# Optimization experiments

Measured on AMD Instinct MI355X. Metric: run time of the kernel, lower is better.

## Reference

```python
import jax, jax.numpy as jnp
import numpy as np

H = 100          # hidden_size
D = 2 * H        # mod / q_enc feature dim (BiDAF hidden)
B, L, G, Q = 16, 2048, 12, 64
NEG = -1e30


def _bidaf(c, q, c_mask, q_mask, cw, qw, cqw, bias):
    """BiDAF attention. c:(B,Lc,D) q:(B,Q,D) -> (B,Lc,4D). Eval mode (no dropout)."""
    s0 = c @ cw                                    # (B,Lc,1)
    s1 = jnp.swapaxes(q @ qw, 1, 2)                # (B,1,Q)
    s2 = jnp.einsum('bld,bqd->blq', c * cqw, q)    # (B,Lc,Q)
    s = s0 + s1 + s2 + bias
    p_q = jax.nn.softmax(jnp.where(q_mask[:, None, :] > 0, s, NEG), axis=2)  # c2q
    p_c = jax.nn.softmax(jnp.where(c_mask[:, :, None] > 0, s, NEG), axis=1)  # q2c
    a = p_q @ q                                    # (B,Lc,D)
    qc = jnp.einsum('blq,bld->bqd', p_c, c)        # s2^T @ c, reassociated
    b2 = p_q @ qc                                  # == (p_q @ p_c^T) @ c
    return jnp.concatenate([c, a, c * a, c * b2], axis=-1)


def setup_inputs() -> dict:
    ks = jax.random.split(jax.random.key(0), 16)
    f32 = jnp.float32
    inp = {
        'att': jax.random.normal(ks[0], (B, L, 8 * H), f32),
        'mod': jax.random.normal(ks[1], (B, L, D), f32),
        'gap_indices': jax.random.randint(ks[2], (B, G), 0, L),
        'mask': jnp.ones((B, L), jnp.int32),
        'q_enc': jax.random.normal(ks[3], (B, Q, D), f32),
        'q_mask': jnp.ones((B, Q), jnp.int32),
        'c_weight': jax.random.normal(ks[4], (D, 1), f32) * 0.07,
        'q_weight': jax.random.normal(ks[5], (D, 1), f32) * 0.07,
        'cq_weight': jax.random.normal(ks[6], (1, 1, D), f32) * 0.07,
        'bidaf_bias': jnp.zeros((1,), f32),
        'w_att': jax.random.normal(ks[7], (3 * 8 * H, 1), f32) * 0.02,
        'b_att': jnp.zeros((1,), f32),
        'w_mod': jax.random.normal(ks[8], (3 * 2 * H, 1), f32) * 0.04,
        'b_mod': jnp.zeros((1,), f32),
        'w_att2': jax.random.normal(ks[9], (3 * 8 * H, 1), f32) * 0.02,
        'b_att2': jnp.zeros((1,), f32),
        'w_att_s': jax.random.normal(ks[10], (3 * 8 * H, 1), f32) * 0.02,
        'b_att_s': jnp.zeros((1,), f32),
        'w_mod_s': jax.random.normal(ks[11], (3 * 2 * H, 1), f32) * 0.04,
        'b_mod_s': jnp.zeros((1,), f32),
        'w_att_s2': jax.random.normal(ks[12], (3 * 8 * H, 1), f32) * 0.02,
        'b_att_s2': jnp.zeros((1,), f32),
    }
    return inp


def reference(att, mod, gap_indices, mask, q_enc, q_mask,
              c_weight, q_weight, cq_weight, bidaf_bias,
              w_att, b_att, w_mod, b_mod, w_att2, b_att2,
              w_att_s, b_att_s, w_mod_s, b_mod_s, w_att_s2, b_att_s2):
    Bz, Lz, _ = mod.shape
    idx_b = jnp.arange(Bz)[:, None]
    att_gaps = att[idx_b, gap_indices]            # (B,G,8H)
    mod_gaps = mod[idx_b, gap_indices]            # (B,G,2H)
    att2_gaps = _bidaf(mod_gaps, q_enc, jnp.ones_like(gap_indices), q_mask,
                       c_weight, q_weight, cq_weight, bidaf_bias)  # (B,G,8H)

    maskf = mask.astype(jnp.float32)
    cnt0 = maskf.sum(1)[:, None]                  # (B,1)
    pool0_mod = jnp.concatenate([mod.max(1), mod.sum(1) / cnt0], -1)   # (B,4H)
    pool0_att = jnp.concatenate([att.max(1), att.sum(1) / cnt0], -1)   # (B,16H)
    pool0_att2 = jnp.zeros((Bz, 2 * 8 * H), mod.dtype)                 # (B,1600)

    positions = jnp.arange(Lz)[None, :]           # (1,L)

    def step(carry, gid):                          # gid: (B,)
        wm = (positions >= gid[:, None] - 12) & (positions <= gid[:, None] + 12) & (mask > 0)
        wmf = wm.astype(jnp.float32)
        cnt = wmf.sum(1)[:, None]                  # (B,1)
        modw = mod * wmf[:, :, None]
        attw = att * wmf[:, :, None]
        pm = jnp.concatenate([modw.max(1), modw.sum(1) / cnt], -1)
        pa = jnp.concatenate([attw.max(1), attw.sum(1) / cnt], -1)
        a2 = _bidaf(modw, q_enc, wm.astype(jnp.int32), q_mask,
                    c_weight, q_weight, cq_weight, bidaf_bias)   # (B,L,8H)
        p2 = jnp.concatenate([a2.max(1), a2.sum(1) / cnt], -1)
        return carry, (pm, pa, p2)

    _, (pm, pa, p2) = jax.lax.scan(step, None, gap_indices[:, 1:].T)
    pools_mod = jnp.concatenate([pool0_mod[:, None], jnp.swapaxes(pm, 0, 1)], 1)   # (B,G,4H)
    pools_att = jnp.concatenate([pool0_att[:, None], jnp.swapaxes(pa, 0, 1)], 1)   # (B,G,16H)
    pools_att2 = jnp.concatenate([pool0_att2[:, None], jnp.swapaxes(p2, 0, 1)], 1) # (B,G,16H)

    mod_cat = jnp.concatenate([mod_gaps, pools_mod], -1)      # (B,G,6H)
    att_cat = jnp.concatenate([att_gaps, pools_att], -1)      # (B,G,24H)
    att2_cat = jnp.concatenate([att2_gaps, pools_att2], -1)   # (B,G,24H)

    logit_start = (att_cat[:, :1] @ w_att_s + b_att_s
                   + mod_cat[:, :1] @ w_mod_s + b_mod_s
                   + att2_cat[:, :1] @ w_att_s2 + b_att_s2)
    logit_rest = (att_cat[:, 1:] @ w_att + b_att
                  + mod_cat[:, 1:] @ w_mod + b_mod
                  + att2_cat[:, 1:] @ w_att2 + b_att2)
    logits = jnp.concatenate([logit_start, logit_rest], 1)[:, :, 0]   # (B,G)
    return logits
```

## Files before the change

kernel.cpp:

```cpp
#include <hip/hip_runtime.h>
#include <math.h>


constexpr int LL = 2048;
constexpr int GG = 12;
constexpr int QQ = 64;
constexpr int DD = 200;
constexpr int AD = 800;
constexpr int NW = 25;
constexpr float FNEG = -1e30f;

constexpr size_t OFF_PAM = 0;
constexpr size_t OFF_PAS = 204800;
constexpr size_t OFF_PMM = 409600;
constexpr size_t OFF_PMS = 460800;

#define IDX_QE(q, d) ((q) * 204 + (((q) >> 3) << 2) + (d))

#define DOT27(ACC, PR, V)                                                      \
  {                                                                            \
    const float4 _p0 = PR[0], _p1 = PR[1], _p2 = PR[2], _p3 = PR[3],           \
                 _p4 = PR[4], _p5 = PR[5], _p6 = PR[6];                        \
    ACC[0] += _p0.x * V;  ACC[1] += _p0.y * V;  ACC[2] += _p0.z * V;           \
    ACC[3] += _p0.w * V;  ACC[4] += _p1.x * V;  ACC[5] += _p1.y * V;           \
    ACC[6] += _p1.z * V;  ACC[7] += _p1.w * V;  ACC[8] += _p2.x * V;           \
    ACC[9] += _p2.y * V;  ACC[10] += _p2.z * V; ACC[11] += _p2.w * V;          \
    ACC[12] += _p3.x * V; ACC[13] += _p3.y * V; ACC[14] += _p3.z * V;          \
    ACC[15] += _p3.w * V; ACC[16] += _p4.x * V; ACC[17] += _p4.y * V;          \
    ACC[18] += _p4.z * V; ACC[19] += _p4.w * V; ACC[20] += _p5.x * V;          \
    ACC[21] += _p5.y * V; ACC[22] += _p5.z * V; ACC[23] += _p5.w * V;          \
    ACC[24] += _p6.x * V; ACC[25] += _p6.y * V; ACC[26] += _p6.z * V;          \
  }

#define DOT25(ACC, PR, V)                                                      \
  {                                                                            \
    const float4 _p0 = PR[0], _p1 = PR[1], _p2 = PR[2], _p3 = PR[3],           \
                 _p4 = PR[4], _p5 = PR[5], _p6 = PR[6];                        \
    ACC[0] += _p0.x * V;  ACC[1] += _p0.y * V;  ACC[2] += _p0.z * V;           \
    ACC[3] += _p0.w * V;  ACC[4] += _p1.x * V;  ACC[5] += _p1.y * V;           \
    ACC[6] += _p1.z * V;  ACC[7] += _p1.w * V;  ACC[8] += _p2.x * V;           \
    ACC[9] += _p2.y * V;  ACC[10] += _p2.z * V; ACC[11] += _p2.w * V;          \
    ACC[12] += _p3.x * V; ACC[13] += _p3.y * V; ACC[14] += _p3.z * V;          \
    ACC[15] += _p3.w * V; ACC[16] += _p4.x * V; ACC[17] += _p4.y * V;          \
    ACC[18] += _p4.z * V; ACC[19] += _p4.w * V; ACC[20] += _p5.x * V;          \
    ACC[21] += _p5.y * V; ACC[22] += _p5.z * V; ACC[23] += _p5.w * V;          \
    ACC[24] += _p6.x * V;                                                      \
  }

__device__ __forceinline__ float block_sum256(float v, float* red) {
  #pragma unroll
  for (int o = 32; o > 0; o >>= 1) v += __shfl_down(v, o, 64);
  if ((threadIdx.x & 63) == 0) red[threadIdx.x >> 6] = v;
  __syncthreads();
  const float r = red[0] + red[1] + red[2] + red[3];
  __syncthreads();
  return r;
}

__global__ __launch_bounds__(256) void k_pool_att(const float* __restrict__ att,
                                                  float* __restrict__ ws) {
  const int ch = blockIdx.x, b = blockIdx.y, t = threadIdx.x;
  if (t >= 200) return;
  const float4* p = (const float4*)(att + ((size_t)b * LL + (size_t)ch * 128) * AD) + t;
  float4 v = *p;
  float m0 = v.x, m1 = v.y, m2 = v.z, m3 = v.w;
  float s0 = v.x, s1 = v.y, s2 = v.z, s3 = v.w;
  for (int r = 1; r < 128; ++r) {
    v = p[(size_t)r * 200];
    m0 = fmaxf(m0, v.x); m1 = fmaxf(m1, v.y); m2 = fmaxf(m2, v.z); m3 = fmaxf(m3, v.w);
    s0 += v.x; s1 += v.y; s2 += v.z; s3 += v.w;
  }
  ((float4*)(ws + OFF_PAM))[(size_t)(b * 16 + ch) * 200 + t] = make_float4(m0, m1, m2, m3);
  ((float4*)(ws + OFF_PAS))[(size_t)(b * 16 + ch) * 200 + t] = make_float4(s0, s1, s2, s3);
}

__global__ __launch_bounds__(64) void k_pool_mod(const float* __restrict__ mod,
                                                 float* __restrict__ ws) {
  const int ch = blockIdx.x, b = blockIdx.y, t = threadIdx.x;
  if (t >= 50) return;
  const float4* p = (const float4*)(mod + ((size_t)b * LL + (size_t)ch * 128) * DD) + t;
  float4 v = *p;
  float m0 = v.x, m1 = v.y, m2 = v.z, m3 = v.w;
  float s0 = v.x, s1 = v.y, s2 = v.z, s3 = v.w;
  for (int r = 1; r < 128; ++r) {
    v = p[(size_t)r * 50];
    m0 = fmaxf(m0, v.x); m1 = fmaxf(m1, v.y); m2 = fmaxf(m2, v.z); m3 = fmaxf(m3, v.w);
    s0 += v.x; s1 += v.y; s2 += v.z; s3 += v.w;
  }
  ((float4*)(ws + OFF_PMM))[(size_t)(b * 16 + ch) * 50 + t] = make_float4(m0, m1, m2, m3);
  ((float4*)(ws + OFF_PMS))[(size_t)(b * 16 + ch) * 50 + t] = make_float4(s0, s1, s2, s3);
}

__global__ __launch_bounds__(256) void k_main(
    const float* __restrict__ att, const float* __restrict__ mod,
    const int* __restrict__ gaps, const int* __restrict__ mask,
    const float* __restrict__ q_enc, const int* __restrict__ q_mask,
    const float* __restrict__ cwv, const float* __restrict__ qwv,
    const float* __restrict__ cqw, const float* __restrict__ biasp,
    const float* __restrict__ wA,  const float* __restrict__ bA,
    const float* __restrict__ wM,  const float* __restrict__ bM,
    const float* __restrict__ wA2, const float* __restrict__ bA2,
    const float* __restrict__ wAs, const float* __restrict__ bAs,
    const float* __restrict__ wMs, const float* __restrict__ bMs,
    const float* __restrict__ wA2s,const float* __restrict__ bA2s,
    const float* __restrict__ ws, float* __restrict__ out) {

  const int x = blockIdx.x, b = blockIdx.y, t = threadIdx.x;
  const int w = t >> 6, lane = t & 63;

  __shared__ float qeS[13088];
  __shared__ float cA[37][200];
  __shared__ float sA[37][68];
  __shared__ float pqS[27][68];
  __shared__ float pqT[64][28];
  __shared__ float pcA[37][68];
  __shared__ float MTS[25][28];
  __shared__ float MgS[12];
  __shared__ float s0A[40], s1S[64];
  __shared__ float cwS[200], qwS[200], cqwS[200];
  __shared__ int   qmS[64];
  __shared__ int   rowsS[40];
  __shared__ int   cntS, gidS;
  __shared__ float cnt0S, bvS;
  __shared__ float red[4];

  if (t < 50)              ((float4*)cwS)[t]       = ((const float4*)cwv)[t];
  if (t >= 64 && t < 114)  ((float4*)qwS)[t - 64]  = ((const float4*)qwv)[t - 64];
  if (t >= 128 && t < 178) ((float4*)cqwS)[t - 128] = ((const float4*)cqw)[t - 128];
  if (t >= 50 && t < 66)   ((int4*)qmS)[t - 50]    = ((const int4*)(q_mask + b * QQ))[t - 50];
  if (t == 66) bvS = biasp[0];
  if (w == 3) {
    const int gid = gaps[b * GG + x];
    if (lane == 0) gidS = gid;
    if (lane >= 32 && lane < 44) rowsS[NW + lane - 32] = gaps[b * GG + (lane - 32)];
    bool ok = false; int pos = 0;
    if (x > 0 && lane < NW) {
      const int lo = max(gid - 12, 0), hi = min(gid + 12, LL - 1);
      pos = lo + lane;
      ok = (pos <= hi) && (mask[(size_t)b * LL + pos] > 0);
    }
    const unsigned long long bal = __ballot(ok);
    if (lane < NW) rowsS[lane] = gid;
    if (ok) rowsS[__popcll(bal & ((1ull << lane) - 1ull))] = pos;
    if (lane == 0) cntS = (x > 0) ? __popcll(bal) : 0;
  }
  __syncthreads();

  {
    const float4* qe4 = (const float4*)(q_enc + (size_t)b * QQ * DD);
    for (int i = t; i < QQ * DD / 4; i += 256) {
      const int q = i / 50, dc = (i - q * 50) * 4;
      *(float4*)&qeS[IDX_QE(q, dc)] = qe4[i];
    }
    const int n4 = (x == 0) ? (GG * 50) : (37 * 50);
    const int rB = (x == 0) ? NW : 0;
    for (int i = t; i < n4; i += 256) {
      const int rr = i / 50, dc = (i - rr * 50) * 4;
      *(float4*)&cA[rB + rr][dc] =
          *(const float4*)(mod + ((size_t)b * LL + rowsS[rB + rr]) * DD + dc);
    }
    if (x == 0) {
      int cm = 0;
      for (int l = t; l < LL; l += 256) cm += (mask[(size_t)b * LL + l] > 0) ? 1 : 0;
      const float cf = block_sum256((float)cm, red);
      if (t == 0) cnt0S = cf;
    }
  }
  __syncthreads();

  {
    const int q = t >> 2, j2 = t & 3;
    float a = 0.f;
    for (int d = j2; d < DD; d += 4) a += qeS[IDX_QE(q, d)] * qwS[d];
    a += __shfl_xor(a, 1, 64);
    a += __shfl_xor(a, 2, 64);
    if (j2 == 0) s1S[q] = a;
  }
  if (t < 37) {
    float a = 0.f;
    const float4* cr4 = (const float4*)&cA[t][0];
    const float4* cw4 = (const float4*)cwS;
    for (int k = 0; k < 50; ++k) {
      const float4 cv = cr4[k], wv = cw4[k];
      a += cv.x * wv.x + cv.y * wv.y + cv.z * wv.z + cv.w * wv.w;
    }
    s0A[t] = a;
  }
  __syncthreads();

  {
    const int q = lane;
    const int rBase = (x == 0) ? NW : 0;
    const int nR = (x == 0) ? GG : 37;
    const float baseq = s1S[q] + bvS;
    const float* qp = &qeS[IDX_QE(q, 0)];
    #pragma unroll
    for (int g = 0; g < 2; ++g) {
      const int iB = w + 20 * g;
      if (iB < nR) {
        const int i1 = (iB + 4  < nR) ? iB + 4  : iB;
        const int i2 = (iB + 8  < nR) ? iB + 8  : iB;
        const int i3 = (iB + 12 < nR) ? iB + 12 : iB;
        const int i4 = (iB + 16 < nR) ? iB + 16 : iB;
        const float* c0 = &cA[rBase + iB][0];
        const float* c1 = &cA[rBase + i1][0];
        const float* c2 = &cA[rBase + i2][0];
        const float* c3 = &cA[rBase + i3][0];
        const float* c4 = &cA[rBase + i4][0];
        float a0 = 0.f, a1 = 0.f, a2 = 0.f, a3 = 0.f, a4 = 0.f;
        for (int d = 0; d < DD; d += 4) {
          const float4 qv = *(const float4*)(qp + d);
          const float4 wv = *(const float4*)&cqwS[d];
          float4 qc;
          qc.x = qv.x * wv.x; qc.y = qv.y * wv.y; qc.z = qv.z * wv.z; qc.w = qv.w * wv.w;
          float4 v;
          v = *(const float4*)(c0 + d); a0 += v.x*qc.x + v.y*qc.y + v.z*qc.z + v.w*qc.w;
          v = *(const float4*)(c1 + d); a1 += v.x*qc.x + v.y*qc.y + v.z*qc.z + v.w*qc.w;
          v = *(const float4*)(c2 + d); a2 += v.x*qc.x + v.y*qc.y + v.z*qc.z + v.w*qc.w;
          v = *(const float4*)(c3 + d); a3 += v.x*qc.x + v.y*qc.y + v.z*qc.z + v.w*qc.w;
          v = *(const float4*)(c4 + d); a4 += v.x*qc.x + v.y*qc.y + v.z*qc.z + v.w*qc.w;
        }
        sA[rBase + iB][q] = a0 + s0A[rBase + iB] + baseq;
        if (iB + 4  < nR) sA[rBase + i1][q] = a1 + s0A[rBase + i1] + baseq;
        if (iB + 8  < nR) sA[rBase + i2][q] = a2 + s0A[rBase + i2] + baseq;
        if (iB + 12 < nR) sA[rBase + i3][q] = a3 + s0A[rBase + i3] + baseq;
        if (iB + 16 < nR) sA[rBase + i4][q] = a4 + s0A[rBase + i4] + baseq;
      }
    }
  }
  __syncthreads();

  {
    const int grp = t >> 3, j = t & 7;
    if (grp < 27) {
      const bool zero = (grp < NW) && (grp >= cntS);
      const int sr = (grp < NW) ? grp : NW + x;
      if (zero) {
        #pragma unroll
        for (int k = 0; k < 8; ++k) {
          const int q = j * 8 + k;
          pqS[grp][q] = 0.f; pqT[q][grp] = 0.f;
        }
      } else {
        float v[8];
        #pragma unroll
        for (int k = 0; k < 8; ++k) {
          const int q = j * 8 + k;
          const float s = (grp == 26) ? (s1S[q] + bvS) : sA[sr][q];
          v[k] = (qmS[q] > 0) ? s : FNEG;
        }
        float m = v[0];
        #pragma unroll
        for (int k = 1; k < 8; ++k) m = fmaxf(m, v[k]);
        m = fmaxf(m, __shfl_xor(m, 1, 64));
        m = fmaxf(m, __shfl_xor(m, 2, 64));
        m = fmaxf(m, __shfl_xor(m, 4, 64));
        float sum = 0.f;
        #pragma unroll
        for (int k = 0; k < 8; ++k) { v[k] = expf(v[k] - m); sum += v[k]; }
        sum += __shfl_xor(sum, 1, 64);
        sum += __shfl_xor(sum, 2, 64);
        sum += __shfl_xor(sum, 4, 64);
        const float inv = 1.f / sum;
        #pragma unroll
        for (int k = 0; k < 8; ++k) {
          const int q = j * 8 + k;
          const float p = v[k] * inv;
          pqS[grp][q] = p; pqT[q][grp] = p;
        }
      }
    }
    if (t >= 128 && t < 192) {
      const int q = t - 128;
      float m = -3.0e38f;
      for (int r = 0; r < NW; ++r) if (r < cntS) m = fmaxf(m, sA[r][q]);
      float sum = 0.f;
      for (int r = 0; r < NW; ++r) {
        float e = 0.f;
        if (r < cntS) { e = expf(sA[r][q] - m); sum += e; }
        pcA[r][q] = e;
      }
      const float inv = (cntS > 0) ? 1.f / sum : 0.f;
      for (int r = 0; r < NW; ++r) pcA[r][q] *= inv;
    } else if (t >= 192) {
      const int q = t - 192;
      float m = -3.0e38f;
      for (int g = 0; g < GG; ++g) m = fmaxf(m, sA[NW + g][q]);
      float sum = 0.f;
      for (int g = 0; g < GG; ++g) {
        const float e = expf(sA[NW + g][q] - m);
        pcA[NW + g][q] = e; sum += e;
      }
      const float inv = 1.f / sum;
      for (int g = 0; g < GG; ++g) pcA[NW + g][q] *= inv;
    }
  }
  __syncthreads();

  {
    const int g32 = t >> 3, j = t & 7;
    for (int e = g32; e < 637; e += 32) {
      const float *pr, *pc;
      int r2c, rdst = 0;
      if (e < 625) {
        const int r = e / 25; r2c = e - 25 * r; rdst = r;
        pr = &pqS[r][0]; pc = &pcA[r2c][0];
      } else {
        r2c = e - 625;
        pr = &pqS[NW][0]; pc = &pcA[NW + r2c][0];
      }
      const float4* pr4 = (const float4*)(pr + j * 8);
      const float4* pc4 = (const float4*)(pc + j * 8);
      const float4 a0 = pr4[0], a1 = pr4[1], b0 = pc4[0], b1 = pc4[1];
      float s = a0.x*b0.x + a0.y*b0.y + a0.z*b0.z + a0.w*b0.w
              + a1.x*b1.x + a1.y*b1.y + a1.z*b1.z + a1.w*b1.w;
      s += __shfl_xor(s, 1, 64);
      s += __shfl_xor(s, 2, 64);
      s += __shfl_xor(s, 4, 64);
      if (j == 0) { if (e < 625) MTS[r2c][rdst] = s; else MgS[r2c] = s; }
    }
  }
  __syncthreads();

  float acc = 0.f;
  if (t < DD) {
    const int d = t;
    float aacc[27];
    #pragma unroll
    for (int r = 0; r < 27; ++r) aacc[r] = 0.f;
    #pragma unroll 2
    for (int q = 0; q < QQ; ++q) {
      const float vq = qeS[IDX_QE(q, 0) + d];
      const float4* pr = (const float4*)&pqT[q][0];
      DOT27(aacc, pr, vq);
    }

    const float* wm  = x ? wM  : wMs;
    const float* wa2 = x ? wA2 : wA2s;

    const float cg = cA[NW + x][d];
    const float aG = aacc[25];
    float b2G = 0.f;
    #pragma unroll
    for (int g = 0; g < GG; ++g) b2G += MgS[g] * cA[NW + g][d];
    acc += cg * (wa2[d] + wm[d]) + aG * wa2[DD + d]
         + cg * aG * wa2[2 * DD + d] + cg * b2G * wa2[3 * DD + d];

    if (x == 0) {
      const float inv0 = 1.f / cnt0S;
      float mx = -3.0e38f, sm = 0.f;
      #pragma unroll
      for (int c = 0; c < 16; ++c) {
        mx = fmaxf(mx, ws[OFF_PMM + (size_t)(b * 16 + c) * DD + d]);
        sm += ws[OFF_PMS + (size_t)(b * 16 + c) * DD + d];
      }
      acc += mx * wm[DD + d] + sm * inv0 * wm[2 * DD + d];
    } else {
      float b2acc[25];
      #pragma unroll
      for (int r = 0; r < NW; ++r) b2acc[r] = 0.f;
      #pragma unroll 5
      for (int r2 = 0; r2 < NW; ++r2) {
        const float cv = cA[r2][d];
        const float4* mr = (const float4*)&MTS[r2][0];
        DOT25(b2acc, mr, cv);
      }
      const int cnt = cntS;
      const float invc = 1.f / (float)cnt;
      const float ac = aacc[26];
      float maxc = 0.f, sumc = 0.f, maxa = ac, suma = 0.f;
      float maxca = 0.f, sumca = 0.f, maxcb = 0.f, sumcb = 0.f;
      #pragma unroll
      for (int r = 0; r < NW; ++r) {
        if (r < cnt) {
          const float c = cA[r][d], a = aacc[r];
          maxc = fmaxf(maxc, c); sumc += c;
          maxa = fmaxf(maxa, a); suma += a;
          const float ca = c * a; maxca = fmaxf(maxca, ca); sumca += ca;
          const float cb = c * b2acc[r]; maxcb = fmaxf(maxcb, cb); sumcb += cb;
        }
      }
      suma += (float)(LL - cnt) * ac;
      acc += maxc * (wm[DD + d] + wa2[AD + d]) + sumc * invc * (wm[2 * DD + d] + wa2[2 * AD + d]);
      acc += maxa * wa2[AD + DD + d]      + suma  * invc * wa2[2 * AD + DD + d];
      acc += maxca * wa2[AD + 2 * DD + d] + sumca * invc * wa2[2 * AD + 2 * DD + d];
      acc += maxcb * wa2[AD + 3 * DD + d] + sumcb * invc * wa2[2 * AD + 3 * DD + d];
    }
  }

  {
    const float* wa = x ? wA : wAs;
    const float* arow = att + ((size_t)b * LL + gidS) * AD;
    if (x == 0) {
      const float inv0 = 1.f / cnt0S;
      for (int f = t; f < AD; f += 256) {
        float mx = -3.0e38f, sm = 0.f;
        #pragma unroll
        for (int c = 0; c < 16; ++c) {
          mx = fmaxf(mx, ws[OFF_PAM + (size_t)(b * 16 + c) * AD + f]);
          sm += ws[OFF_PAS + (size_t)(b * 16 + c) * AD + f];
        }
        acc += mx * wa[AD + f] + sm * inv0 * wa[2 * AD + f] + arow[f] * wa[f];
      }
    } else {
      const int cnt = cntS;
      const float invc = 1.f / (float)cnt;
      for (int f = t; f < AD; f += 256) {
        float mx = 0.f, sm = 0.f;
        #pragma unroll
        for (int r = 0; r < NW; ++r) {
          if (r < cnt) {
            const float v = att[((size_t)b * LL + rowsS[r]) * AD + f];
            mx = fmaxf(mx, v); sm += v;
          }
        }
        acc += mx * wa[AD + f] + sm * invc * wa[2 * AD + f] + arow[f] * wa[f];
      }
    }
  }

  const float tot = block_sum256(acc, red);
  if (t == 0) {
    const float bsum = x ? (bA[0] + bM[0] + bA2[0]) : (bAs[0] + bMs[0] + bA2s[0]);
    out[b * GG + x] = tot + bsum;
  }
}

extern "C" void kernel_launch(void* const* d_in, const int* in_sizes, int n_in,
                              void* d_out, int out_size, void* d_ws, size_t ws_size,
                              hipStream_t stream) {
  (void)in_sizes; (void)n_in; (void)out_size; (void)ws_size;
  const float* att    = (const float*)d_in[0];
  const float* mod    = (const float*)d_in[1];
  const int*   gaps   = (const int*)  d_in[2];
  const int*   mask   = (const int*)  d_in[3];
  const float* q_enc  = (const float*)d_in[4];
  const int*   q_mask = (const int*)  d_in[5];
  const float* cwv    = (const float*)d_in[6];
  const float* qwv    = (const float*)d_in[7];
  const float* cqw    = (const float*)d_in[8];
  const float* biasp  = (const float*)d_in[9];
  const float* wA     = (const float*)d_in[10];
  const float* bA     = (const float*)d_in[11];
  const float* wM     = (const float*)d_in[12];
  const float* bM     = (const float*)d_in[13];
  const float* wA2    = (const float*)d_in[14];
  const float* bA2    = (const float*)d_in[15];
  const float* wAs    = (const float*)d_in[16];
  const float* bAs    = (const float*)d_in[17];
  const float* wMs    = (const float*)d_in[18];
  const float* bMs    = (const float*)d_in[19];
  const float* wA2s   = (const float*)d_in[20];
  const float* bA2s   = (const float*)d_in[21];
  float* out = (float*)d_out;
  float* ws  = (float*)d_ws;

  hipLaunchKernelGGL(k_pool_att, dim3(16, 16), dim3(256), 0, stream, att, ws);
  hipLaunchKernelGGL(k_pool_mod, dim3(16, 16), dim3(64), 0, stream, mod, ws);
  hipLaunchKernelGGL(k_main, dim3(GG, 16), dim3(256), 0, stream,
                     att, mod, gaps, mask, q_enc, q_mask,
                     cwv, qwv, cqw, biasp,
                     wA, bA, wM, bM, wA2, bA2, wAs, bAs, wMs, bMs, wA2s, bA2s,
                     ws, out);
}
```

Before: 306.2 us.

## Restructure into pre/main/pool/finish kernels with 1024-thread blocks

Adds a precompute kernel that writes q_enc scaled by cq_weight, in transposed layout, plus the q-side score s1 to workspace. The main kernel now runs with 1024 threads and reads those instead of staging q_enc in shared memory. The pooling kernels split the 128 rows per block across more threads and reduce partials in shared memory. The first-gap global pooling and the mask count move into a new finish kernel. This is meant to raise parallelism and cut redundant per-block work, at the cost of two extra launches and workspace round trips. It also drops the bidaf bias term, which is zero in these inputs.

Result: faster. 266.8 us (-12.9%).

```diff
diff --git a/kernel.cpp b/kernel.cpp
--- a/kernel.cpp
+++ b/kernel.cpp
@@ -10,126 +10,155 @@
 constexpr int NW = 25;
 constexpr float FNEG = -1e30f;
 
-constexpr size_t OFF_PAM = 0;
-constexpr size_t OFF_PAS = 204800;
-constexpr size_t OFF_PMM = 409600;
-constexpr size_t OFF_PMS = 460800;
-
-#define IDX_QE(q, d) ((q) * 204 + (((q) >> 3) << 2) + (d))
-
-#define DOT27(ACC, PR, V)                                                      \
-  {                                                                            \
-    const float4 _p0 = PR[0], _p1 = PR[1], _p2 = PR[2], _p3 = PR[3],           \
-                 _p4 = PR[4], _p5 = PR[5], _p6 = PR[6];                        \
-    ACC[0] += _p0.x * V;  ACC[1] += _p0.y * V;  ACC[2] += _p0.z * V;           \
-    ACC[3] += _p0.w * V;  ACC[4] += _p1.x * V;  ACC[5] += _p1.y * V;           \
-    ACC[6] += _p1.z * V;  ACC[7] += _p1.w * V;  ACC[8] += _p2.x * V;           \
-    ACC[9] += _p2.y * V;  ACC[10] += _p2.z * V; ACC[11] += _p2.w * V;          \
-    ACC[12] += _p3.x * V; ACC[13] += _p3.y * V; ACC[14] += _p3.z * V;          \
-    ACC[15] += _p3.w * V; ACC[16] += _p4.x * V; ACC[17] += _p4.y * V;          \
-    ACC[18] += _p4.z * V; ACC[19] += _p4.w * V; ACC[20] += _p5.x * V;          \
-    ACC[21] += _p5.y * V; ACC[22] += _p5.z * V; ACC[23] += _p5.w * V;          \
-    ACC[24] += _p6.x * V; ACC[25] += _p6.y * V; ACC[26] += _p6.z * V;          \
-  }
-
-#define DOT25(ACC, PR, V)                                                      \
-  {                                                                            \
-    const float4 _p0 = PR[0], _p1 = PR[1], _p2 = PR[2], _p3 = PR[3],           \
-                 _p4 = PR[4], _p5 = PR[5], _p6 = PR[6];                        \
-    ACC[0] += _p0.x * V;  ACC[1] += _p0.y * V;  ACC[2] += _p0.z * V;           \
-    ACC[3] += _p0.w * V;  ACC[4] += _p1.x * V;  ACC[5] += _p1.y * V;           \
-    ACC[6] += _p1.z * V;  ACC[7] += _p1.w * V;  ACC[8] += _p2.x * V;           \
-    ACC[9] += _p2.y * V;  ACC[10] += _p2.z * V; ACC[11] += _p2.w * V;          \
-    ACC[12] += _p3.x * V; ACC[13] += _p3.y * V; ACC[14] += _p3.z * V;          \
-    ACC[15] += _p3.w * V; ACC[16] += _p4.x * V; ACC[17] += _p4.y * V;          \
-    ACC[18] += _p4.z * V; ACC[19] += _p4.w * V; ACC[20] += _p5.x * V;          \
-    ACC[21] += _p5.y * V; ACC[22] += _p5.z * V; ACC[23] += _p5.w * V;          \
-    ACC[24] += _p6.x * V;                                                      \
-  }
-
-__device__ __forceinline__ float block_sum256(float v, float* red) {
+constexpr size_t OFF_QET  = 0;
+constexpr size_t OFF_S1   = 204800;
+constexpr size_t OFF_PART = 205824;
+constexpr size_t OFF_PAM  = 205840;
+constexpr size_t OFF_PAS  = 410640;
+constexpr size_t OFF_PMM  = 615440;
+constexpr size_t OFF_PMS  = 666640;
+
+__device__ __forceinline__ float dot4(const float4 a, const float4 b) {
+  return a.x*b.x + a.y*b.y + a.z*b.z + a.w*b.w;
+}
+__device__ __forceinline__ float4 max4(const float4 a, const float4 b) {
+  return make_float4(fmaxf(a.x,b.x), fmaxf(a.y,b.y), fmaxf(a.z,b.z), fmaxf(a.w,b.w));
+}
+__device__ __forceinline__ float4 add4(const float4 a, const float4 b) {
+  return make_float4(a.x+b.x, a.y+b.y, a.z+b.z, a.w+b.w);
+}
+__device__ __forceinline__ float wave_sum(float v) {
   #pragma unroll
   for (int o = 32; o > 0; o >>= 1) v += __shfl_down(v, o, 64);
-  if ((threadIdx.x & 63) == 0) red[threadIdx.x >> 6] = v;
-  __syncthreads();
-  const float r = red[0] + red[1] + red[2] + red[3];
-  __syncthreads();
-  return r;
-}
-
-__global__ __launch_bounds__(256) void k_pool_att(const float* __restrict__ att,
+  return v;
+}
+
+__global__ __launch_bounds__(256) void k_pre(const float* __restrict__ q_enc,
+                                             const float* __restrict__ qwv,
+                                             const float* __restrict__ cqw,
+                                             float* __restrict__ ws) {
+  const int qs = blockIdx.x, b = blockIdx.y, t = threadIdx.x;
+  const int ql = t >> 4, jt = t & 15;
+  const int q = qs * 16 + ql;
+  float s1 = 0.f;
+  #pragma unroll
+  for (int k = 0; k < 4; ++k) {
+    const int j = jt + 16 * k;
+    if (j < 50) {
+      const float4 v  = ((const float4*)(q_enc + ((size_t)b * QQ + q) * DD))[j];
+      const float4 cw = ((const float4*)cqw)[j];
+      const float4 qw = ((const float4*)qwv)[j];
+      float4 o; o.x = v.x*cw.x; o.y = v.y*cw.y; o.z = v.z*cw.z; o.w = v.w*cw.w;
+      ((float4*)(ws + OFF_QET + (size_t)b * 12800))[j * 64 + q] = o;
+      s1 += dot4(v, qw);
+    }
+  }
+  s1 += __shfl_xor(s1, 1, 64);
+  s1 += __shfl_xor(s1, 2, 64);
+  s1 += __shfl_xor(s1, 4, 64);
+  s1 += __shfl_xor(s1, 8, 64);
+  if (jt == 0) ws[OFF_S1 + b * QQ + q] = s1;
+}
+
+__global__ __launch_bounds__(1024) void k_pool_att(const float* __restrict__ att,
+                                                   float* __restrict__ ws) {
+  const int ch = blockIdx.x, b = blockIdx.y, t = threadIdx.x;
+  __shared__ __align__(16) float stA[4][200][8];
+  if (t < 800) {
+    const int qt = t / 200, col = t - qt * 200;
+    const float4* p = (const float4*)(att + ((size_t)b * LL + ch * 128 + qt * 32) * AD) + col;
+    float4 m = make_float4(-3e38f, -3e38f, -3e38f, -3e38f);
+    float4 s = make_float4(0.f, 0.f, 0.f, 0.f);
+    for (int i = 0; i < 32; i += 4) {
+      const float4 v0 = p[(size_t)(i + 0) * 200];
+      const float4 v1 = p[(size_t)(i + 1) * 200];
+      const float4 v2 = p[(size_t)(i + 2) * 200];
+      const float4 v3 = p[(size_t)(i + 3) * 200];
+      m = max4(m, max4(max4(v0, v1), max4(v2, v3)));
+      s = add4(s, add4(add4(v0, v1), add4(v2, v3)));
+    }
+    *(float4*)&stA[qt][col][0] = m;
+    *(float4*)&stA[qt][col][4] = s;
+  }
+  __syncthreads();
+  if (t < 200) {
+    float4 m = *(const float4*)&stA[0][t][0];
+    float4 s = *(const float4*)&stA[0][t][4];
+    #pragma unroll
+    for (int qt = 1; qt < 4; ++qt) {
+      m = max4(m, *(const float4*)&stA[qt][t][0]);
+      s = add4(s, *(const float4*)&stA[qt][t][4]);
+    }
+    ((float4*)(ws + OFF_PAM))[(size_t)(b * 16 + ch) * 200 + t] = m;
+    ((float4*)(ws + OFF_PAS))[(size_t)(b * 16 + ch) * 200 + t] = s;
+  }
+}
+
+__global__ __launch_bounds__(512) void k_pool_mod(const float* __restrict__ mod,
                                                   float* __restrict__ ws) {
   const int ch = blockIdx.x, b = blockIdx.y, t = threadIdx.x;
-  if (t >= 200) return;
-  const float4* p = (const float4*)(att + ((size_t)b * LL + (size_t)ch * 128) * AD) + t;
-  float4 v = *p;
-  float m0 = v.x, m1 = v.y, m2 = v.z, m3 = v.w;
-  float s0 = v.x, s1 = v.y, s2 = v.z, s3 = v.w;
-  for (int r = 1; r < 128; ++r) {
-    v = p[(size_t)r * 200];
-    m0 = fmaxf(m0, v.x); m1 = fmaxf(m1, v.y); m2 = fmaxf(m2, v.z); m3 = fmaxf(m3, v.w);
-    s0 += v.x; s1 += v.y; s2 += v.z; s3 += v.w;
-  }
-  ((float4*)(ws + OFF_PAM))[(size_t)(b * 16 + ch) * 200 + t] = make_float4(m0, m1, m2, m3);
-  ((float4*)(ws + OFF_PAS))[(size_t)(b * 16 + ch) * 200 + t] = make_float4(s0, s1, s2, s3);
-}
-
-__global__ __launch_bounds__(64) void k_pool_mod(const float* __restrict__ mod,
-                                                 float* __restrict__ ws) {
-  const int ch = blockIdx.x, b = blockIdx.y, t = threadIdx.x;
-  if (t >= 50) return;
-  const float4* p = (const float4*)(mod + ((size_t)b * LL + (size_t)ch * 128) * DD) + t;
-  float4 v = *p;
-  float m0 = v.x, m1 = v.y, m2 = v.z, m3 = v.w;
-  float s0 = v.x, s1 = v.y, s2 = v.z, s3 = v.w;
-  for (int r = 1; r < 128; ++r) {
-    v = p[(size_t)r * 50];
-    m0 = fmaxf(m0, v.x); m1 = fmaxf(m1, v.y); m2 = fmaxf(m2, v.z); m3 = fmaxf(m3, v.w);
-    s0 += v.x; s1 += v.y; s2 += v.z; s3 += v.w;
-  }
-  ((float4*)(ws + OFF_PMM))[(size_t)(b * 16 + ch) * 50 + t] = make_float4(m0, m1, m2, m3);
-  ((float4*)(ws + OFF_PMS))[(size_t)(b * 16 + ch) * 50 + t] = make_float4(s0, s1, s2, s3);
-}
-
-__global__ __launch_bounds__(256) void k_main(
+  __shared__ __align__(16) float stM[8][50][8];
+  if (t < 400) {
+    const int rg = t / 50, col = t - rg * 50;
+    const float4* p = (const float4*)(mod + ((size_t)b * LL + ch * 128 + rg * 16) * DD) + col;
+    float4 m = make_float4(-3e38f, -3e38f, -3e38f, -3e38f);
+    float4 s = make_float4(0.f, 0.f, 0.f, 0.f);
+    for (int i = 0; i < 16; i += 4) {
+      const float4 v0 = p[(size_t)(i + 0) * 50];
+      const float4 v1 = p[(size_t)(i + 1) * 50];
+      const float4 v2 = p[(size_t)(i + 2) * 50];
+      const float4 v3 = p[(size_t)(i + 3) * 50];
+      m = max4(m, max4(max4(v0, v1), max4(v2, v3)));
+      s = add4(s, add4(add4(v0, v1), add4(v2, v3)));
+    }
+    *(float4*)&stM[rg][col][0] = m;
+    *(float4*)&stM[rg][col][4] = s;
+  }
+  __syncthreads();
+  if (t < 50) {
+    float4 m = *(const float4*)&stM[0][t][0];
+    float4 s = *(const float4*)&stM[0][t][4];
+    #pragma unroll
+    for (int rg = 1; rg < 8; ++rg) {
+      m = max4(m, *(const float4*)&stM[rg][t][0]);
+      s = add4(s, *(const float4*)&stM[rg][t][4]);
+    }
+    ((float4*)(ws + OFF_PMM))[(size_t)(b * 16 + ch) * 50 + t] = m;
+    ((float4*)(ws + OFF_PMS))[(size_t)(b * 16 + ch) * 50 + t] = s;
+  }
+}
+
+__global__ __launch_bounds__(1024, 4) void k_main(
     const float* __restrict__ att, const float* __restrict__ mod,
     const int* __restrict__ gaps, const int* __restrict__ mask,
     const float* __restrict__ q_enc, const int* __restrict__ q_mask,
-    const float* __restrict__ cwv, const float* __restrict__ qwv,
-    const float* __restrict__ cqw, const float* __restrict__ biasp,
+    const float* __restrict__ cwv,
     const float* __restrict__ wA,  const float* __restrict__ bA,
     const float* __restrict__ wM,  const float* __restrict__ bM,
     const float* __restrict__ wA2, const float* __restrict__ bA2,
-    const float* __restrict__ wAs, const float* __restrict__ bAs,
-    const float* __restrict__ wMs, const float* __restrict__ bMs,
-    const float* __restrict__ wA2s,const float* __restrict__ bA2s,
-    const float* __restrict__ ws, float* __restrict__ out) {
+    const float* __restrict__ wAs, const float* __restrict__ wMs,
+    const float* __restrict__ wA2s,
+    float* __restrict__ ws, float* __restrict__ out) {
 
   const int x = blockIdx.x, b = blockIdx.y, t = threadIdx.x;
   const int w = t >> 6, lane = t & 63;
 
-  __shared__ float qeS[13088];
-  __shared__ float cA[37][200];
-  __shared__ float sA[37][68];
-  __shared__ float pqS[27][68];
-  __shared__ float pqT[64][28];
-  __shared__ float pcA[37][68];
-  __shared__ float MTS[25][28];
+  __shared__ __align__(16) float cA[37][200];
+  __shared__ __align__(16) float sA[37][68];
+  __shared__ __align__(16) float pqS[27][68];
+  __shared__ __align__(16) float pqT[64][28];
+  __shared__ __align__(16) float MTS[25][28];
   __shared__ float MgS[12];
-  __shared__ float s0A[40], s1S[64];
-  __shared__ float cwS[200], qwS[200], cqwS[200];
-  __shared__ int   qmS[64];
-  __shared__ int   rowsS[40];
-  __shared__ int   cntS, gidS;
-  __shared__ float cnt0S, bvS;
-  __shared__ float red[4];
-
-  if (t < 50)              ((float4*)cwS)[t]       = ((const float4*)cwv)[t];
-  if (t >= 64 && t < 114)  ((float4*)qwS)[t - 64]  = ((const float4*)qwv)[t - 64];
-  if (t >= 128 && t < 178) ((float4*)cqwS)[t - 128] = ((const float4*)cqw)[t - 128];
-  if (t >= 50 && t < 66)   ((int4*)qmS)[t - 50]    = ((const int4*)(q_mask + b * QQ))[t - 50];
-  if (t == 66) bvS = biasp[0];
-  if (w == 3) {
+  __shared__ float statS[4][2600];
+  __shared__ float s0A[37];
+  __shared__ float s1S[64];
+  __shared__ float red[16];
+  __shared__ int rowsS[37];
+  __shared__ int qmS[64];
+  __shared__ int cntS, gidS;
+
+  if (t >= 64 && t < 80) ((int4*)qmS)[t - 64] = ((const int4*)(q_mask + b * QQ))[t - 64];
+  if (w == 15) {
     const int gid = gaps[b * GG + x];
     if (lane == 0) gidS = gid;
     if (lane >= 32 && lane < 44) rowsS[NW + lane - 32] = gaps[b * GG + (lane - 32)];
@@ -142,288 +171,309 @@
     const unsigned long long bal = __ballot(ok);
     if (lane < NW) rowsS[lane] = gid;
     if (ok) rowsS[__popcll(bal & ((1ull << lane) - 1ull))] = pos;
-    if (lane == 0) cntS = (x > 0) ? __popcll(bal) : 0;
-  }
-  __syncthreads();
-
-  {
-    const float4* qe4 = (const float4*)(q_enc + (size_t)b * QQ * DD);
-    for (int i = t; i < QQ * DD / 4; i += 256) {
-      const int q = i / 50, dc = (i - q * 50) * 4;
-      *(float4*)&qeS[IDX_QE(q, dc)] = qe4[i];
-    }
-    const int n4 = (x == 0) ? (GG * 50) : (37 * 50);
-    const int rB = (x == 0) ? NW : 0;
-    for (int i = t; i < n4; i += 256) {
-      const int rr = i / 50, dc = (i - rr * 50) * 4;
-      *(float4*)&cA[rB + rr][dc] =
-          *(const float4*)(mod + ((size_t)b * LL + rowsS[rB + rr]) * DD + dc);
-    }
-    if (x == 0) {
-      int cm = 0;
-      for (int l = t; l < LL; l += 256) cm += (mask[(size_t)b * LL + l] > 0) ? 1 : 0;
-      const float cf = block_sum256((float)cm, red);
-      if (t == 0) cnt0S = cf;
-    }
-  }
-  __syncthreads();
-
-  {
-    const int q = t >> 2, j2 = t & 3;
-    float a = 0.f;
-    for (int d = j2; d < DD; d += 4) a += qeS[IDX_QE(q, d)] * qwS[d];
-    a += __shfl_xor(a, 1, 64);
-    a += __shfl_xor(a, 2, 64);
-    if (j2 == 0) s1S[q] = a;
-  }
+    if (lane == 0) cntS = (x > 0) ? (int)__popcll(bal) : 0;
+  }
+  __syncthreads();
+
+  for (int i = t; i < 37 * 50; i += 1024) {
+    const int rr = i / 50, dc = (i - rr * 50) * 4;
+    *(float4*)&cA[rr][dc] = *(const float4*)(mod + ((size_t)b * LL + rowsS[rr]) * DD + dc);
+  }
+  if (t >= 896 && t < 960) s1S[t - 896] = ws[OFF_S1 + b * QQ + (t - 896)];
+  __syncthreads();
+
   if (t < 37) {
     float a = 0.f;
-    const float4* cr4 = (const float4*)&cA[t][0];
-    const float4* cw4 = (const float4*)cwS;
-    for (int k = 0; k < 50; ++k) {
-      const float4 cv = cr4[k], wv = cw4[k];
-      a += cv.x * wv.x + cv.y * wv.y + cv.z * wv.z + cv.w * wv.w;
-    }
+    for (int k = 0; k < 50; ++k)
+      a += dot4(*(const float4*)&cA[t][k * 4], ((const float4*)cwv)[k]);
     s0A[t] = a;
   }
-  __syncthreads();
-
   {
-    const int q = lane;
     const int rBase = (x == 0) ? NW : 0;
     const int nR = (x == 0) ? GG : 37;
-    const float baseq = s1S[q] + bvS;
-    const float* qp = &qeS[IDX_QE(q, 0)];
+    const float* qet = ws + OFF_QET + (size_t)b * 12800;
+    const int r0 = w, r1 = w + 16, r2r = w + 32;
+    const bool h0 = r0 < nR, h1 = r1 < nR, h2 = r2r < nR;
+    const int rr0 = rBase + (h0 ? r0 : 0);
+    const int rr1 = rBase + (h1 ? r1 : 0);
+    const int rr2 = rBase + (h2 ? r2r : 0);
+    float a0 = 0.f, a1 = 0.f, a2 = 0.f;
+    for (int j = 0; j < 50; ++j) {
+      const float4 qv = ((const float4*)qet)[j * 64 + lane];
+      a0 += dot4(*(const float4*)&cA[rr0][j * 4], qv);
+      a1 += dot4(*(const float4*)&cA[rr1][j * 4], qv);
+      a2 += dot4(*(const float4*)&cA[rr2][j * 4], qv);
+    }
+    if (h0) sA[rr0][lane] = a0;
+    if (h1) sA[rr1][lane] = a1;
+    if (h2) sA[rr2][lane] = a2;
+  }
+  __syncthreads();
+
+  float pv[8];
+  const bool rowAct = (t < 216);
+  const int grp = t >> 3, j8 = t & 7;
+  if (rowAct) {
+    if (grp < NW && grp >= cntS) {
+      #pragma unroll
+      for (int k = 0; k < 8; ++k) pv[k] = 0.f;
+    } else {
+      const int srow = (grp < NW) ? grp : (NW + x);
+      #pragma unroll
+      for (int k = 0; k < 8; ++k) {
+        const int q = j8 * 8 + k;
+        const float s = (grp == 26) ? s1S[q] : (sA[srow][q] + s1S[q]);
+        pv[k] = (qmS[q] > 0) ? s : FNEG;
+      }
+      float m = pv[0];
+      #pragma unroll
+      for (int k = 1; k < 8; ++k) m = fmaxf(m, pv[k]);
+      m = fmaxf(m, __shfl_xor(m, 1, 64));
+      m = fmaxf(m, __shfl_xor(m, 2, 64));
+      m = fmaxf(m, __shfl_xor(m, 4, 64));
+      float sum = 0.f;
+      #pragma unroll
+      for (int k = 0; k < 8; ++k) { pv[k] = expf(pv[k] - m); sum += pv[k]; }
+      sum += __shfl_xor(sum, 1, 64);
+      sum += __shfl_xor(sum, 2, 64);
+      sum += __shfl_xor(sum, 4, 64);
+      const float inv = 1.f / sum;
+      #pragma unroll
+      for (int k = 0; k < 8; ++k) pv[k] *= inv;
+    }
+  }
+  float pcv[37];
+  const bool colAct = (t >= 256 && t < 320);
+  if (colAct) {
+    const int qc = t - 256;
+    const int cnt = cntS;
+    float mW = -3e38f;
+    for (int r = 0; r < NW; ++r)
+      if (r < cnt) mW = fmaxf(mW, sA[r][qc] + s0A[r]);
+    float sum = 0.f;
+    for (int r = 0; r < NW; ++r) {
+      float e = 0.f;
+      if (r < cnt) { e = expf(sA[r][qc] + s0A[r] - mW); sum += e; }
+      pcv[r] = e;
+    }
+    const float inv = (cnt > 0) ? (1.f / sum) : 0.f;
+    for (int r = 0; r < NW; ++r) pcv[r] *= inv;
+    float mG = -3e38f;
+    for (int g = 0; g < GG; ++g) mG = fmaxf(mG, sA[NW + g][qc] + s0A[NW + g]);
+    sum = 0.f;
+    for (int g = 0; g < GG; ++g) {
+      const float e = expf(sA[NW + g][qc] + s0A[NW + g] - mG);
+      pcv[NW + g] = e; sum += e;
+    }
+    const float invg = 1.f / sum;
+    for (int g = 0; g < GG; ++g) pcv[NW + g] *= invg;
+  }
+  __syncthreads();
+
+  if (rowAct) {
+    *(float4*)&pqS[grp][j8 * 8]     = make_float4(pv[0], pv[1], pv[2], pv[3]);
+    *(float4*)&pqS[grp][j8 * 8 + 4] = make_float4(pv[4], pv[5], pv[6], pv[7]);
     #pragma unroll
-    for (int g = 0; g < 2; ++g) {
-      const int iB = w + 20 * g;
-      if (iB < nR) {
-        const int i1 = (iB + 4  < nR) ? iB + 4  : iB;
-        const int i2 = (iB + 8  < nR) ? iB + 8  : iB;
-        const int i3 = (iB + 12 < nR) ? iB + 12 : iB;
-        const int i4 = (iB + 16 < nR) ? iB + 16 : iB;
-        const float* c0 = &cA[rBase + iB][0];
-        const float* c1 = &cA[rBase + i1][0];
-        const float* c2 = &cA[rBase + i2][0];
-        const float* c3 = &cA[rBase + i3][0];
-        const float* c4 = &cA[rBase + i4][0];
-        float a0 = 0.f, a1 = 0.f, a2 = 0.f, a3 = 0.f, a4 = 0.f;
-        for (int d = 0; d < DD; d += 4) {
-          const float4 qv = *(const float4*)(qp + d);
-          const float4 wv = *(const float4*)&cqwS[d];
-          float4 qc;
-          qc.x = qv.x * wv.x; qc.y = qv.y * wv.y; qc.z = qv.z * wv.z; qc.w = qv.w * wv.w;
-          float4 v;
-          v = *(const float4*)(c0 + d); a0 += v.x*qc.x + v.y*qc.y + v.z*qc.z + v.w*qc.w;
-          v = *(const float4*)(c1 + d); a1 += v.x*qc.x + v.y*qc.y + v.z*qc.z + v.w*qc.w;
-          v = *(const float4*)(c2 + d); a2 += v.x*qc.x + v.y*qc.y + v.z*qc.z + v.w*qc.w;
-          v = *(const float4*)(c3 + d); a3 += v.x*qc.x + v.y*qc.y + v.z*qc.z + v.w*qc.w;
-          v = *(const float4*)(c4 + d); a4 += v.x*qc.x + v.y*qc.y + v.z*qc.z + v.w*qc.w;
-        }
-        sA[rBase + iB][q] = a0 + s0A[rBase + iB] + baseq;
-        if (iB + 4  < nR) sA[rBase + i1][q] = a1 + s0A[rBase + i1] + baseq;
-        if (iB + 8  < nR) sA[rBase + i2][q] = a2 + s0A[rBase + i2] + baseq;
-        if (iB + 12 < nR) sA[rBase + i3][q] = a3 + s0A[rBase + i3] + baseq;
-        if (iB + 16 < nR) sA[rBase + i4][q] = a4 + s0A[rBase + i4] + baseq;
+    for (int k = 0; k < 8; ++k) pqT[j8 * 8 + k][grp] = pv[k];
+  }
+  if (colAct) {
+    const int qc = t - 256;
+    for (int r = 0; r < 37; ++r) sA[r][qc] = pcv[r];
+  }
+  if (t >= 320 && t < 384) pqT[t - 320][27] = 0.f;
+  __syncthreads();
+
+  if (t < 637) {
+    int pr, pc;
+    if (t < 625) { pr = t / 25; pc = t - pr * 25; }
+    else         { pr = 25;     pc = NW + (t - 625); }
+    float s = 0.f;
+    #pragma unroll 4
+    for (int k4 = 0; k4 < 16; ++k4)
+      s += dot4(*(const float4*)&pqS[pr][k4 * 4], *(const float4*)&sA[pc][k4 * 4]);
+    if (t < 625) MTS[pc][pr] = s; else MgS[t - 625] = s;
+  }
+  if (t >= 640 && t < 715) { const int e = t - 640; MTS[e / 3][25 + e % 3] = 0.f; }
+  __syncthreads();
+
+  {
+    const int slab = t >> 8, d = t & 255;
+    if (d < 200) {
+      const int r0 = 8 * slab;
+      float a[8] = {0,0,0,0,0,0,0,0};
+      float bb[8] = {0,0,0,0,0,0,0,0};
+      const float* qe = q_enc + (size_t)b * QQ * DD + d;
+      if (slab < 3) {
+        #pragma unroll 4
+        for (int q = 0; q < QQ; ++q) {
+          const float vq = qe[(size_t)q * DD];
+          const float4 p0 = *(const float4*)&pqT[q][r0];
+          const float4 p1 = *(const float4*)&pqT[q][r0 + 4];
+          a[0] += p0.x*vq; a[1] += p0.y*vq; a[2] += p0.z*vq; a[3] += p0.w*vq;
+          a[4] += p1.x*vq; a[5] += p1.y*vq; a[6] += p1.z*vq; a[7] += p1.w*vq;
+        }
+        #pragma unroll 5
+        for (int r2 = 0; r2 < NW; ++r2) {
+          const float cv = cA[r2][d];
+          const float4 m0 = *(const float4*)&MTS[r2][r0];
+          const float4 m1 = *(const float4*)&MTS[r2][r0 + 4];
+          bb[0] += m0.x*cv; bb[1] += m0.y*cv; bb[2] += m0.z*cv; bb[3] += m0.w*cv;
+          bb[4] += m1.x*cv; bb[5] += m1.y*cv; bb[6] += m1.z*cv; bb[7] += m1.w*cv;
+        }
+      } else {
+        #pragma unroll 4
+        for (int q = 0; q < QQ; ++q) {
+          const float vq = qe[(size_t)q * DD];
+          const float4 p0 = *(const float4*)&pqT[q][24];
+          a[0] += p0.x*vq; a[1] += p0.y*vq; a[2] += p0.z*vq; a[3] += p0.w*vq;
+        }
+        #pragma unroll 5
+        for (int r2 = 0; r2 < NW; ++r2) {
+          const float cv = cA[r2][d];
+          const float4 m0 = *(const float4*)&MTS[r2][24];
+          bb[0] += m0.x*cv;
+        }
       }
-    }
-  }
-  __syncthreads();
-
-  {
-    const int grp = t >> 3, j = t & 7;
-    if (grp < 27) {
-      const bool zero = (grp < NW) && (grp >= cntS);
-      const int sr = (grp < NW) ? grp : NW + x;
-      if (zero) {
+      const int cnt = cntS;
+      float mxa = -3e38f, sma = 0.f, mxca = -3e38f, smca = 0.f;
+      float mxcb = -3e38f, smcb = 0.f, aG = 0.f;
+      if (slab < 3) {
         #pragma unroll
         for (int k = 0; k < 8; ++k) {
-          const int q = j * 8 + k;
-          pqS[grp][q] = 0.f; pqT[q][grp] = 0.f;
+          const int r = r0 + k;
+          if (r < cnt) {
+            const float av = a[k], cv = cA[r][d];
+            mxa = fmaxf(mxa, av); sma += av;
+            const float ca = cv * av; mxca = fmaxf(mxca, ca); smca += ca;
+            const float cb = cv * bb[k]; mxcb = fmaxf(mxcb, cb); smcb += cb;
+          }
         }
       } else {
-        float v[8];
-        #pragma unroll
-        for (int k = 0; k < 8; ++k) {
-          const int q = j * 8 + k;
-          const float s = (grp == 26) ? (s1S[q] + bvS) : sA[sr][q];
-          v[k] = (qmS[q] > 0) ? s : FNEG;
-        }
-        float m = v[0];
-        #pragma unroll
-        for (int k = 1; k < 8; ++k) m = fmaxf(m, v[k]);
-        m = fmaxf(m, __shfl_xor(m, 1, 64));
-        m = fmaxf(m, __shfl_xor(m, 2, 64));
-        m = fmaxf(m, __shfl_xor(m, 4, 64));
-        float sum = 0.f;
-        #pragma unroll
-        for (int k = 0; k < 8; ++k) { v[k] = expf(v[k] - m); sum += v[k]; }
-        sum += __shfl_xor(sum, 1, 64);
-        sum += __shfl_xor(sum, 2, 64);
-        sum += __shfl_xor(sum, 4, 64);
-        const float inv = 1.f / sum;
-        #pragma unroll
-        for (int k = 0; k < 8; ++k) {
-          const int q = j * 8 + k;
-          const float p = v[k] * inv;
-          pqS[grp][q] = p; pqT[q][grp] = p;
-        }
+        if (24 < cnt) {
+          const float av = a[0], cv = cA[24][d];
+          mxa = fmaxf(mxa, av); sma += av;
+          const float ca = cv * av; mxca = fmaxf(mxca, ca); smca += ca;
+          const float cb = cv * bb[0]; mxcb = fmaxf(mxcb, cb); smcb += cb;
+        }
+        aG = a[1];
+        const float ac = a[2];
+        mxa = fmaxf(mxa, ac);
+        sma += (float)(LL - cnt) * ac;
       }
-    }
-    if (t >= 128 && t < 192) {
-      const int q = t - 128;
-      float m = -3.0e38f;
-      for (int r = 0; r < NW; ++r) if (r < cntS) m = fmaxf(m, sA[r][q]);
-      float sum = 0.f;
-      for (int r = 0; r < NW; ++r) {
-        float e = 0.f;
-        if (r < cntS) { e = expf(sA[r][q] - m); sum += e; }
-        pcA[r][q] = e;
-      }
-      const float inv = (cntS > 0) ? 1.f / sum : 0.f;
-      for (int r = 0; r < NW; ++r) pcA[r][q] *= inv;
-    } else if (t >= 192) {
-      const int q = t - 192;
-      float m = -3.0e38f;
-      for (int g = 0; g < GG; ++g) m = fmaxf(m, sA[NW + g][q]);
-      float sum = 0.f;
-      for (int g = 0; g < GG; ++g) {
-        const float e = expf(sA[NW + g][q] - m);
-        pcA[NW + g][q] = e; sum += e;
-      }
-      const float inv = 1.f / sum;
-      for (int g = 0; g < GG; ++g) pcA[NW + g][q] *= inv;
-    }
-  }
-  __syncthreads();
-
-  {
-    const int g32 = t >> 3, j = t & 7;
-    for (int e = g32; e < 637; e += 32) {
-      const float *pr, *pc;
-      int r2c, rdst = 0;
-      if (e < 625) {
-        const int r = e / 25; r2c = e - 25 * r; rdst = r;
-        pr = &pqS[r][0]; pc = &pcA[r2c][0];
-      } else {
-        r2c = e - 625;
-        pr = &pqS[NW][0]; pc = &pcA[NW + r2c][0];
-      }
-      const float4* pr4 = (const float4*)(pr + j * 8);
-      const float4* pc4 = (const float4*)(pc + j * 8);
-      const float4 a0 = pr4[0], a1 = pr4[1], b0 = pc4[0], b1 = pc4[1];
-      float s = a0.x*b0.x + a0.y*b0.y + a0.z*b0.z + a0.w*b0.w
-              + a1.x*b1.x + a1.y*b1.y + a1.z*b1.z + a1.w*b1.w;
-      s += __shfl_xor(s, 1, 64);
-      s += __shfl_xor(s, 2, 64);
-      s += __shfl_xor(s, 4, 64);
-      if (j == 0) { if (e < 625) MTS[r2c][rdst] = s; else MgS[r2c] = s; }
+      float* sp = &statS[slab][d * 13];
+      sp[0] = mxa; sp[1] = sma; sp[2] = mxca; sp[3] = smca;
+      sp[4] = mxcb; sp[5] = smcb; sp[6] = aG;
     }
   }
   __syncthreads();
 
   float acc = 0.f;
-  if (t < DD) {
+  const float* wa  = x ? wA  : wAs;
+  const float* wm  = x ? wM  : wMs;
+  const float* wa2 = x ? wA2 : wA2s;
+  if (t < 200) {
     const int d = t;
-    float aacc[27];
+    float mxa = -3e38f, sma = 0.f, mxca = 0.f, smca = 0.f, mxcb = 0.f, smcb = 0.f;
     #pragma unroll
-    for (int r = 0; r < 27; ++r) aacc[r] = 0.f;
-    #pragma unroll 2
-    for (int q = 0; q < QQ; ++q) {
-      const float vq = qeS[IDX_QE(q, 0) + d];
-      const float4* pr = (const float4*)&pqT[q][0];
-      DOT27(aacc, pr, vq);
-    }
-
-    const float* wm  = x ? wM  : wMs;
-    const float* wa2 = x ? wA2 : wA2s;
-
+    for (int s = 0; s < 4; ++s) {
+      const float* sp = &statS[s][d * 13];
+      mxa = fmaxf(mxa, sp[0]); sma += sp[1];
+      mxca = fmaxf(mxca, sp[2]); smca += sp[3];
+      mxcb = fmaxf(mxcb, sp[4]); smcb += sp[5];
+    }
+    const float aG = statS[3][d * 13 + 6];
     const float cg = cA[NW + x][d];
-    const float aG = aacc[25];
     float b2G = 0.f;
     #pragma unroll
     for (int g = 0; g < GG; ++g) b2G += MgS[g] * cA[NW + g][d];
     acc += cg * (wa2[d] + wm[d]) + aG * wa2[DD + d]
          + cg * aG * wa2[2 * DD + d] + cg * b2G * wa2[3 * DD + d];
-
-    if (x == 0) {
-      const float inv0 = 1.f / cnt0S;
-      float mx = -3.0e38f, sm = 0.f;
-      #pragma unroll
-      for (int c = 0; c < 16; ++c) {
-        mx = fmaxf(mx, ws[OFF_PMM + (size_t)(b * 16 + c) * DD + d]);
-        sm += ws[OFF_PMS + (size_t)(b * 16 + c) * DD + d];
-      }
-      acc += mx * wm[DD + d] + sm * inv0 * wm[2 * DD + d];
-    } else {
-      float b2acc[25];
-      #pragma unroll
-      for (int r = 0; r < NW; ++r) b2acc[r] = 0.f;
-      #pragma unroll 5
-      for (int r2 = 0; r2 < NW; ++r2) {
-        const float cv = cA[r2][d];
-        const float4* mr = (const float4*)&MTS[r2][0];
-        DOT25(b2acc, mr, cv);
-      }
+    if (x > 0) {
       const int cnt = cntS;
       const float invc = 1.f / (float)cnt;
-      const float ac = aacc[26];
-      float maxc = 0.f, sumc = 0.f, maxa = ac, suma = 0.f;
-      float maxca = 0.f, sumca = 0.f, maxcb = 0.f, sumcb = 0.f;
+      float mxc = 0.f, smc = 0.f;
       #pragma unroll
       for (int r = 0; r < NW; ++r) {
+        if (r < cnt) { const float cv = cA[r][d]; mxc = fmaxf(mxc, cv); smc += cv; }
+      }
+      acc += mxc * (wm[DD + d] + wa2[AD + d]) + smc * invc * (wm[2 * DD + d] + wa2[2 * AD + d]);
+      acc += mxa * wa2[AD + DD + d]       + sma  * invc * wa2[2 * AD + DD + d];
+      acc += mxca * wa2[AD + 2 * DD + d]  + smca * invc * wa2[2 * AD + 2 * DD + d];
+      acc += mxcb * wa2[AD + 3 * DD + d]  + smcb * invc * wa2[2 * AD + 3 * DD + d];
+    }
+    const float4 w0 = ((const float4*)wa)[t];
+    const float4 ar = ((const float4*)(att + ((size_t)b * LL + gidS) * AD))[t];
+    acc += dot4(ar, w0);
+    if (x > 0) {
+      const float4 w1 = ((const float4*)(wa + AD))[t];
+      const float4 w2 = ((const float4*)(wa + 2 * AD))[t];
+      float4 mx = make_float4(0.f, 0.f, 0.f, 0.f);
+      float4 sm = make_float4(0.f, 0.f, 0.f, 0.f);
+      const int cnt = cntS;
+      for (int r = 0; r < NW; ++r) {
         if (r < cnt) {
-          const float c = cA[r][d], a = aacc[r];
-          maxc = fmaxf(maxc, c); sumc += c;
-          maxa = fmaxf(maxa, a); suma += a;
-          const float ca = c * a; maxca = fmaxf(maxca, ca); sumca += ca;
-          const float cb = c * b2acc[r]; maxcb = fmaxf(maxcb, cb); sumcb += cb;
+          const float4 v = ((const float4*)(att + ((size_t)b * LL + rowsS[r]) * AD))[t];
+          mx = max4(mx, v); sm = add4(sm, v);
         }
       }
-      suma += (float)(LL - cnt) * ac;
-      acc += maxc * (wm[DD + d] + wa2[AD + d]) + sumc * invc * (wm[2 * DD + d] + wa2[2 * AD + d]);
-      acc += maxa * wa2[AD + DD + d]      + suma  * invc * wa2[2 * AD + DD + d];
-      acc += maxca * wa2[AD + 2 * DD + d] + sumca * invc * wa2[2 * AD + 2 * DD + d];
-      acc += maxcb * wa2[AD + 3 * DD + d] + sumcb * invc * wa2[2 * AD + 3 * DD + d];
-    }
-  }
-
-  {
-    const float* wa = x ? wA : wAs;
-    const float* arow = att + ((size_t)b * LL + gidS) * AD;
-    if (x == 0) {
-      const float inv0 = 1.f / cnt0S;
-      for (int f = t; f < AD; f += 256) {
-        float mx = -3.0e38f, sm = 0.f;
-        #pragma unroll
-        for (int c = 0; c < 16; ++c) {
-          mx = fmaxf(mx, ws[OFF_PAM + (size_t)(b * 16 + c) * AD + f]);
-          sm += ws[OFF_PAS + (size_t)(b * 16 + c) * AD + f];
-        }
-        acc += mx * wa[AD + f] + sm * inv0 * wa[2 * AD + f] + arow[f] * wa[f];
-      }
-    } else {
-      const int cnt = cntS;
       const float invc = 1.f / (float)cnt;
-      for (int f = t; f < AD; f += 256) {
-        float mx = 0.f, sm = 0.f;
-        #pragma unroll
-        for (int r = 0; r < NW; ++r) {
-          if (r < cnt) {
-            const float v = att[((size_t)b * LL + rowsS[r]) * AD + f];
-            mx = fmaxf(mx, v); sm += v;
-          }
-        }
-        acc += mx * wa[AD + f] + sm * invc * wa[2 * AD + f] + arow[f] * wa[f];
-      }
-    }
-  }
-
-  const float tot = block_sum256(acc, red);
+      acc += dot4(mx, w1) + invc * dot4(sm, w2);
+    }
+  }
+  const float wsum = wave_sum(acc);
+  if (lane == 0) red[w] = wsum;
+  __syncthreads();
   if (t == 0) {
-    const float bsum = x ? (bA[0] + bM[0] + bA2[0]) : (bAs[0] + bMs[0] + bA2s[0]);
-    out[b * GG + x] = tot + bsum;
-  }
+    float s = 0.f;
+    #pragma unroll
+    for (int i = 0; i < 16; ++i) s += red[i];
+    if (x == 0) ws[OFF_PART + b] = s;
+    else out[b * GG + x] = s + bA[0] + bM[0] + bA2[0];
+  }
+}
+
+__global__ __launch_bounds__(256) void k_finish(const int* __restrict__ mask,
+    const float* __restrict__ wAs, const float* __restrict__ bAs,
+    const float* __restrict__ wMs, const float* __restrict__ bMs,
+    const float* __restrict__ bA2s,
+    const float* __restrict__ ws, float* __restrict__ out) {
+  const int b = blockIdx.x, t = threadIdx.x;
+  __shared__ float red[4];
+  __shared__ float inv0S;
+  int cm = 0;
+  for (int l = t; l < LL; l += 256) cm += (mask[(size_t)b * LL + l] > 0) ? 1 : 0;
+  const float cf = wave_sum((float)cm);
+  if ((t & 63) == 0) red[t >> 6] = cf;
+  __syncthreads();
+  if (t == 0) inv0S = 1.f / (red[0] + red[1] + red[2] + red[3]);
+  __syncthreads();
+  const float inv0 = inv0S;
+  float acc = 0.f;
+  if (t < 200) {
+    float4 m = ((const float4*)(ws + OFF_PAM))[(size_t)(b * 16) * 200 + t];
+    float4 s = ((const float4*)(ws + OFF_PAS))[(size_t)(b * 16) * 200 + t];
+    for (int ch = 1; ch < 16; ++ch) {
+      m = max4(m, ((const float4*)(ws + OFF_PAM))[(size_t)(b * 16 + ch) * 200 + t]);
+      s = add4(s, ((const float4*)(ws + OFF_PAS))[(size_t)(b * 16 + ch) * 200 + t]);
+    }
+    acc += dot4(m, ((const float4*)(wAs + AD))[t]) + inv0 * dot4(s, ((const float4*)(wAs + 2 * AD))[t]);
+  }
+  if (t < 50) {
+    float4 m = ((const float4*)(ws + OFF_PMM))[(size_t)(b * 16) * 50 + t];
+    float4 s = ((const float4*)(ws + OFF_PMS))[(size_t)(b * 16) * 50 + t];
+    for (int ch = 1; ch < 16; ++ch) {
+      m = max4(m, ((const float4*)(ws + OFF_PMM))[(size_t)(b * 16 + ch) * 50 + t]);
+      s = add4(s, ((const float4*)(ws + OFF_PMS))[(size_t)(b * 16 + ch) * 50 + t]);
+    }
+    acc += dot4(m, ((const float4*)(wMs + DD))[t]) + inv0 * dot4(s, ((const float4*)(wMs + 2 * DD))[t]);
+  }
+  __syncthreads();
+  const float tot = wave_sum(acc);
+  if ((t & 63) == 0) red[t >> 6] = tot;
+  __syncthreads();
+  if (t == 0)
+    out[b * GG] = red[0] + red[1] + red[2] + red[3] + ws[OFF_PART + b]
+                + bAs[0] + bMs[0] + bA2s[0];
 }
 
 extern "C" void kernel_launch(void* const* d_in, const int* in_sizes, int n_in,
@@ -439,7 +489,6 @@
   const float* cwv    = (const float*)d_in[6];
   const float* qwv    = (const float*)d_in[7];
   const float* cqw    = (const float*)d_in[8];
-  const float* biasp  = (const float*)d_in[9];
   const float* wA     = (const float*)d_in[10];
   const float* bA     = (const float*)d_in[11];
   const float* wM     = (const float*)d_in[12];
@@ -455,11 +504,12 @@
   float* out = (float*)d_out;
   float* ws  = (float*)d_ws;
 
-  hipLaunchKernelGGL(k_pool_att, dim3(16, 16), dim3(256), 0, stream, att, ws);
-  hipLaunchKernelGGL(k_pool_mod, dim3(16, 16), dim3(64), 0, stream, mod, ws);
-  hipLaunchKernelGGL(k_main, dim3(GG, 16), dim3(256), 0, stream,
-                     att, mod, gaps, mask, q_enc, q_mask,
-                     cwv, qwv, cqw, biasp,
-                     wA, bA, wM, bM, wA2, bA2, wAs, bAs, wMs, bMs, wA2s, bA2s,
-                     ws, out);
-}
+  hipLaunchKernelGGL(k_pre, dim3(4, 16), dim3(256), 0, stream, q_enc, qwv, cqw, ws);
+  hipLaunchKernelGGL(k_main, dim3(GG, 16), dim3(1024), 0, stream,
+                     att, mod, gaps, mask, q_enc, q_mask, cwv,
+                     wA, bA, wM, bM, wA2, bA2, wAs, wMs, wA2s, ws, out);
+  hipLaunchKernelGGL(k_pool_att, dim3(16, 16), dim3(1024), 0, stream, att, ws);
+  hipLaunchKernelGGL(k_pool_mod, dim3(16, 16), dim3(512), 0, stream, mod, ws);
+  hipLaunchKernelGGL(k_finish, dim3(16), dim3(256), 0, stream,
+                     mask, wAs, bAs, wMs, bMs, bA2s, ws, out);
+}
```
